# Kernel tuning notes

Measured on AMD Instinct MI355X. Metric: run time of the kernel, lower is better.

## Reference

```python
import jax, jax.numpy as jnp
import numpy as np
import math

IN_FEATURES = 4096
OUT_FEATURES = 4096
TOKENS = 8192


def hydrate_weight(seed, out_features, in_features):
    """Deterministically synthesize the virtual weight matrix from the 64-bit seed.
    Mirrors nn.Linear's kaiming-uniform-style bound (1/sqrt(fan_in)) used by gmem_rs
    hydration; never stored as a parameter."""
    bound = 1.0 / math.sqrt(in_features)
    key = jax.random.key(seed)
    return jax.random.uniform(
        key, (out_features, in_features), dtype=jnp.float32,
        minval=-bound, maxval=bound)


def setup_inputs() -> dict:
    key = jax.random.key(0)
    kx, kb = jax.random.split(key)
    x = jax.random.normal(kx, (TOKENS, IN_FEATURES), dtype=jnp.float32)
    bound = 1.0 / math.sqrt(IN_FEATURES)
    bias = jax.random.uniform(kb, (OUT_FEATURES,), dtype=jnp.float32,
                              minval=-bound, maxval=bound)
    return {"x": x, "bias": bias, "seed": 1140071481}


def reference(x, bias, seed):
    # Hydrate weight on-the-fly from seed (zero-RAM virtual weight), then GEMM.
    W = hydrate_weight(seed, OUT_FEATURES, IN_FEATURES)  # [out, in]
    y = jnp.einsum('ti,oi->to', x, W)  # [tokens, out]
    return y + bias
```

## Files before the change

kernel.cpp:

```cpp
#include <hip/hip_runtime.h>
#include <hip/hip_bf16.h>
#include <stdint.h>

#define TOKENS 8192
#define NOUT   4096
#define KIN    4096

#define BM 256
#define BN 256
#define BK 64
#define NT (KIN / BK)

typedef __attribute__((ext_vector_type(8))) short bf16x8;
typedef __attribute__((ext_vector_type(4))) float f32x4;

__device__ __forceinline__ uint32_t rotl32(uint32_t x, int r) {
  return (x << r) | (x >> (32 - r));
}

__device__ __forceinline__ uint16_t f2bf_rne(float f) {
  uint32_t u = __float_as_uint(f);
  u += 0x7FFFu + ((u >> 16) & 1u);
  return (uint16_t)(u >> 16);
}

__device__ __forceinline__ void threefry2x32(uint32_t k0, uint32_t k1,
                                             uint32_t c0, uint32_t c1,
                                             uint32_t& o0, uint32_t& o1) {
  uint32_t ks2 = 0x1BD11BDAu ^ k0 ^ k1;
  uint32_t x0 = c0 + k0;
  uint32_t x1 = c1 + k1;
#define TFR(r) { x0 += x1; x1 = rotl32(x1, (r)); x1 ^= x0; }
  TFR(13) TFR(15) TFR(26) TFR(6)
  x0 += k1;  x1 += ks2 + 1u;
  TFR(17) TFR(29) TFR(16) TFR(24)
  x0 += ks2; x1 += k0 + 2u;
  TFR(13) TFR(15) TFR(26) TFR(6)
  x0 += k0;  x1 += k1 + 3u;
  TFR(17) TFR(29) TFR(16) TFR(24)
  x0 += k1;  x1 += ks2 + 4u;
  TFR(13) TFR(15) TFR(26) TFR(6)
  x0 += ks2; x1 += k0 + 5u;
#undef TFR
  o0 = x0; o1 = x1;
}

__global__ void prep_kernel(const float* __restrict__ x,
                            uint16_t* __restrict__ xb,
                            uint16_t* __restrict__ W,
                            const int* __restrict__ seed_ptr) {
  uint32_t b = blockIdx.x;
  uint32_t g = b / 3u, r = b % 3u;
  if (r == 0u) {
    uint32_t k1 = (uint32_t)(*seed_ptr);
    uint32_t j0 = (g * 256u + threadIdx.x) * 8u;
    const float scale = 0.03125f;
    const float mn    = -0.015625f;
    union { uint16_t u[8]; bf16x8 v; } rr;
#pragma unroll
    for (int e = 0; e < 8; ++e) {
      uint32_t o0, o1;
      threefry2x32(0u, k1, 0u, j0 + (uint32_t)e, o0, o1);
      uint32_t bits = o0 ^ o1;
      float f = __uint_as_float((bits >> 9) | 0x3F800000u) - 1.0f;
      float v = fmaxf(mn, f * scale + mn);
      rr.u[e] = f2bf_rne(v);
    }
    *(bf16x8*)(W + j0) = rr.v;
  } else {
    uint32_t cg = g * 2u + (r - 1u);
    uint32_t base = (cg * 256u + threadIdx.x) * 8u;
    f32x4 a = __builtin_nontemporal_load((const f32x4*)(x + base));
    f32x4 c = __builtin_nontemporal_load((const f32x4*)(x + base + 4));
    union { uint16_t u[8]; bf16x8 v; } rr;
    rr.u[0] = f2bf_rne(a[0]); rr.u[1] = f2bf_rne(a[1]);
    rr.u[2] = f2bf_rne(a[2]); rr.u[3] = f2bf_rne(a[3]);
    rr.u[4] = f2bf_rne(c[0]); rr.u[5] = f2bf_rne(c[1]);
    rr.u[6] = f2bf_rne(c[2]); rr.u[7] = f2bf_rne(c[3]);
    *(bf16x8*)(xb + base) = rr.v;
  }
}

__global__ __launch_bounds__(512, 2)
void gemm_bias_kernel(const uint16_t* __restrict__ A,
                      const uint16_t* __restrict__ B,
                      const float* __restrict__ bias,
                      float* __restrict__ C) {
  __shared__ uint16_t smem[2][2][16384];

  const int nwgn = NOUT / BN;
  const int nwg  = (TOKENS / BM) * nwgn;
  int bid = blockIdx.x;
  int cpx = nwg >> 3;
  int swzb = (bid & 7) * cpx + (bid >> 3);
  const int tm = (swzb / nwgn) * BM;
  const int tn = (swzb % nwgn) * BN;

  const int t    = threadIdx.x;
  const int lane = t & 63;
  const int wid  = t >> 6;
  const int wm   = wid >> 2;
  const int wn   = wid & 3;
  const int fr   = lane & 15;
  const int fq   = lane >> 4;

  const int swzRd = (lane & 7) << 4;
  const int lsw   = ((lane & 7) ^ (lane >> 3)) << 4;

  const char* sA  = (const char*)(A + (size_t)(tm + wid * 16 + (lane >> 3)) * KIN) + lsw;
  const char* sB  = (const char*)(B + (size_t)(tn + wid * 16 + (lane >> 3)) * KIN) + lsw;
  const char* sA1 = sA + (size_t)128 * KIN * 2;
  const char* sB1 = sB + (size_t)128 * KIN * 2;

  char* const smemB = (char*)&smem[0][0][0];
  char* const dstB  = smemB + wid * 2048 + lane * 16;

  const int rA00 = (wm * 64 + fr) * 128 + ((fq << 4) ^ swzRd);
  const int rA01 = rA00 ^ 64;
  const int rA10 = rA00 + 65536;
  const int rA11 = rA10 ^ 64;
  const int rB00 = 32768 + (wn * 32 + fr) * 128 + ((fq << 4) ^ swzRd);
  const int rB01 = rB00 ^ 64;
  const int rB10 = rB00 + 65536;
  const int rB11 = rB10 ^ 64;

  f32x4 acc[8][4] = {};
  bf16x8 af[2][4], bv0[2][2], bv1[2][2];

  auto stage2 = [&](const char* src, char* dst) {
    __builtin_amdgcn_global_load_lds(
        (const __attribute__((address_space(1))) void*)src,
        (__attribute__((address_space(3))) void*)dst, 16, 0, 0);
    __builtin_amdgcn_global_load_lds(
        (const __attribute__((address_space(1))) void*)(src + (size_t)8 * KIN * 2),
        (__attribute__((address_space(3))) void*)(dst + 1024), 16, 0, 0);
  };

#define VMW(N) asm volatile("s_waitcnt vmcnt(" #N ")" ::: "memory")
#define LKW(N) asm volatile("s_waitcnt lgkmcnt(" #N ")" ::: "memory")
#define SB0    __builtin_amdgcn_sched_barrier(0)
#define PRI(p) __builtin_amdgcn_s_setprio(p)

#define RD_A4(BASE, S)                                                         \
    _Pragma("unroll")                                                          \
    for (int i_ = 0; i_ < 4; ++i_)                                             \
      af[S][i_] = *(const bf16x8*)(smemB + (BASE) + i_ * 2048);

#define RD_B2(BASE, BV, S)                                                     \
    _Pragma("unroll")                                                          \
    for (int j_ = 0; j_ < 2; ++j_)                                             \
      BV[S][j_] = *(const bf16x8*)(smemB + (BASE) + j_ * 2048);

#define MF8(MH, NH, BV, S)                                                     \
    _Pragma("unroll")                                                          \
    for (int i_ = 0; i_ < 4; ++i_)                                             \
      _Pragma("unroll")                                                        \
      for (int j_ = 0; j_ < 2; ++j_)                                           \
        acc[(MH) * 4 + i_][(NH) * 2 + j_] =                                    \
            __builtin_amdgcn_mfma_f32_16x16x32_bf16(                           \
                af[S][i_], BV[S][j_], acc[(MH) * 4 + i_][(NH) * 2 + j_],       \
                0, 0, 0);

#define KTILE(BUF, OFF1, OFF2, MODE)                                           \
  {                                                                            \
                       \
    RD_A4((BUF) ? rA10 : rA00, 0) RD_B2((BUF) ? rB10 : rB00, bv0, 0)           \
    SB0;                                                                       \
    RD_A4((BUF) ? rA11 : rA01, 1) RD_B2((BUF) ? rB11 : rB01, bv0, 1)           \
    if ((MODE) <= 1) stage2(sA1 + (OFF1),                                      \
                            dstB + ((BUF) ^ 1) * 65536 + 16384);               \
    LKW(8);                                                                    \
    __builtin_amdgcn_s_barrier();                                              \
    LKW(6); SB0; PRI(1); MF8(0, 0, bv0, 0)                                     \
    LKW(0); SB0; MF8(0, 0, bv0, 1) PRI(0);                                     \
                                                   \
    RD_B2(((BUF) ? rB10 : rB00) + 16384, bv1, 0)                               \
    SB0;                                                                       \
    RD_B2(((BUF) ? rB11 : rB01) + 16384, bv1, 1)                               \
    LKW(2);                                                                    \
    __builtin_amdgcn_s_barrier();                                              \
    LKW(2); SB0; PRI(1); MF8(0, 1, bv1, 0)                                     \
    LKW(0); SB0; MF8(0, 1, bv1, 1) PRI(0);                                     \
            \
    RD_A4(((BUF) ? rA10 : rA00) + 16384, 0)                                    \
    SB0;                                                                       \
    RD_A4(((BUF) ? rA11 : rA01) + 16384, 1)                                    \
    if ((MODE) == 0) { stage2(sA + (OFF2), dstB + (BUF) * 65536);              \
                       stage2(sB + (OFF2), dstB + (BUF) * 65536 + 32768); }    \
    LKW(4);                                                                    \
    __builtin_amdgcn_s_barrier();                                              \
    LKW(4); SB0; PRI(1); MF8(1, 1, bv1, 0)                                     \
    LKW(0); SB0; MF8(1, 1, bv1, 1) PRI(0);                                     \
        \
    if ((MODE) == 0) stage2(sB1 + (OFF2), dstB + (BUF) * 65536 + 49152);       \
    if ((MODE) == 0) { VMW(6); } else if ((MODE) == 1) { VMW(0); }             \
    __builtin_amdgcn_s_barrier();                                              \
    SB0; PRI(1); MF8(1, 0, bv0, 0) MF8(1, 0, bv0, 1) PRI(0);                   \
  }

  stage2(sA,        dstB);
  stage2(sB,        dstB + 32768);
  stage2(sA1,       dstB + 16384);
  stage2(sB1,       dstB + 49152);
  stage2(sA  + 128, dstB + 65536);
  stage2(sB  + 128, dstB + 65536 + 32768);
  stage2(sB1 + 128, dstB + 65536 + 49152);
  VMW(6);
  __builtin_amdgcn_s_barrier();

  for (int it = 0; it < (NT - 2) / 2; ++it) {
    KTILE(0, 128, 256, 0)
    KTILE(1, 256, 384, 0)
    sA += 256; sB += 256; sA1 += 256; sB1 += 256;
  }
  KTILE(0, 128, 0, 1)
  KTILE(1, 0, 0, 2)

#undef KTILE
#undef MF8
#undef RD_B2
#undef RD_A4
#undef PRI
#undef SB0
#undef LKW
#undef VMW

  __builtin_amdgcn_s_barrier();
  float* const eb = (float*)(smemB + wid * 4608);
  const int erow = lane >> 3;
  const int ecol = (lane & 7) * 4;
#pragma unroll
  for (int mh = 0; mh < 2; ++mh) {
#pragma unroll
    for (int nh = 0; nh < 2; ++nh) {
#pragma unroll
      for (int c = 0; c < 2; ++c) {
#pragma unroll
        for (int i2 = 0; i2 < 2; ++i2)
#pragma unroll
          for (int j = 0; j < 2; ++j)
#pragma unroll
            for (int rr = 0; rr < 4; ++rr)
              eb[(i2 * 16 + fq * 4 + rr) * 36 + j * 16 + fr] =
                  acc[mh * 4 + c * 2 + i2][nh * 2 + j][rr] +
                  bias[tn + wn * 32 + nh * 128 + j * 16 + fr];
        __builtin_amdgcn_s_waitcnt(0);
        const size_t rbase = (size_t)(tm + wm * 64 + mh * 128 + c * 32 + erow);
        float* cp = C + rbase * NOUT + tn + wn * 32 + nh * 128 + ecol;
#pragma unroll
        for (int rb = 0; rb < 4; ++rb) {
          f32x4 v = *(const f32x4*)(eb + (rb * 8 + erow) * 36 + ecol);
          __builtin_nontemporal_store(v, (f32x4*)(cp + (size_t)rb * 8 * NOUT));
        }
        __builtin_amdgcn_s_waitcnt(0);
      }
    }
  }
}

extern "C" void kernel_launch(void* const* d_in, const int* in_sizes, int n_in,
                              void* d_out, int out_size, void* d_ws, size_t ws_size,
                              hipStream_t stream) {
  const float* x    = (const float*)d_in[0];
  const float* bias = (const float*)d_in[1];
  const int*   seed = (const int*)d_in[2];
  float* y = (float*)d_out;

  uint16_t* Wb = (uint16_t*)d_ws;
  uint16_t* Xb = Wb + (size_t)NOUT * KIN;

  prep_kernel<<<24576, 256, 0, stream>>>(x, Xb, Wb, seed);

  const int grid = (TOKENS / BM) * (NOUT / BN);
  gemm_bias_kernel<<<grid, 512, 0, stream>>>(Xb, Wb, bias, y);
}
```

Before: 247.6 us.

## Switch GEMM to 4 waves with 128x128 per-wave tiles and simpler pipeline

Restructures the 256x256 GEMM tile to use 256 threads (4 waves, 2x2) where each wave computes a 128x128 sub-tile with 64 accumulators, instead of 8 waves with 64x64-ish sub-tiles. The staging and compute schedule is simplified: loads are issued in bulk after barriers with full lgkmcnt/vmcnt waits, and the setprio and fine-grained interleaving are dropped. Bias values are hoisted into registers for the epilogue. This raises register pressure heavily (256 accumulator floats per lane) and lowers occupancy, risking spills and less latency hiding.

Measured after the change: 327.9 us. 32.4% more time.

```diff
diff --git a/kernel.cpp b/kernel.cpp
--- a/kernel.cpp
+++ b/kernel.cpp
@@ -81,7 +81,7 @@
   }
 }
 
-__global__ __launch_bounds__(512, 2)
+__global__ __launch_bounds__(256, 1)
 void gemm_bias_kernel(const uint16_t* __restrict__ A,
                       const uint16_t* __restrict__ B,
                       const float* __restrict__ bias,
@@ -99,161 +99,139 @@
   const int t    = threadIdx.x;
   const int lane = t & 63;
   const int wid  = t >> 6;
-  const int wm   = wid >> 2;
-  const int wn   = wid & 3;
+  const int wm   = wid >> 1;
+  const int wn   = wid & 1;
   const int fr   = lane & 15;
   const int fq   = lane >> 4;
 
   const int swzRd = (lane & 7) << 4;
-  const int lsw   = ((lane & 7) ^ (lane >> 3)) << 4;
-
-  const char* sA  = (const char*)(A + (size_t)(tm + wid * 16 + (lane >> 3)) * KIN) + lsw;
-  const char* sB  = (const char*)(B + (size_t)(tn + wid * 16 + (lane >> 3)) * KIN) + lsw;
-  const char* sA1 = sA + (size_t)128 * KIN * 2;
-  const char* sB1 = sB + (size_t)128 * KIN * 2;
+  const int lsw   = ((t & 7) ^ ((t >> 3) & 7)) << 4;
+
+  const char* sA = (const char*)(A + (size_t)(tm + (t >> 3)) * KIN) + lsw;
+  const char* sB = (const char*)(B + (size_t)(tn + (t >> 3)) * KIN) + lsw;
 
   char* const smemB = (char*)&smem[0][0][0];
-  char* const dstB  = smemB + wid * 2048 + lane * 16;
-
-  const int rA00 = (wm * 64 + fr) * 128 + ((fq << 4) ^ swzRd);
-  const int rA01 = rA00 ^ 64;
-  const int rA10 = rA00 + 65536;
-  const int rA11 = rA10 ^ 64;
-  const int rB00 = 32768 + (wn * 32 + fr) * 128 + ((fq << 4) ^ swzRd);
-  const int rB01 = rB00 ^ 64;
-  const int rB10 = rB00 + 65536;
-  const int rB11 = rB10 ^ 64;
-
-  f32x4 acc[8][4] = {};
-  bf16x8 af[2][4], bv0[2][2], bv1[2][2];
-
-  auto stage2 = [&](const char* src, char* dst) {
+  char* const dstT  = smemB + t * 16;
+
+  const int rA0 = (wm * 128 + fr) * 128 + ((fq << 4) ^ swzRd);
+  const int rB0 = 32768 + (wn * 128 + fr) * 128 + ((fq << 4) ^ swzRd);
+
+  f32x4 acc[8][8] = {};
+  bf16x8 af[8], bv[8];
+
+  auto g1 = [&](const char* src, char* dst) {
     __builtin_amdgcn_global_load_lds(
         (const __attribute__((address_space(1))) void*)src,
         (__attribute__((address_space(3))) void*)dst, 16, 0, 0);
-    __builtin_amdgcn_global_load_lds(
-        (const __attribute__((address_space(1))) void*)(src + (size_t)8 * KIN * 2),
-        (__attribute__((address_space(3))) void*)(dst + 1024), 16, 0, 0);
+  };
+  auto stA = [&](int buf, int off) {
+#pragma unroll
+    for (int q = 0; q < 8; ++q)
+      g1(sA + (size_t)q * 262144 + off, dstT + buf * 65536 + q * 4096);
+  };
+  auto stB = [&](int buf, int off, int q0, int q1) {
+#pragma unroll
+    for (int q = 0; q < 8; ++q)
+      if (q >= q0 && q <= q1)
+        g1(sB + (size_t)q * 262144 + off, dstT + buf * 65536 + 32768 + q * 4096);
   };
 
 #define VMW(N) asm volatile("s_waitcnt vmcnt(" #N ")" ::: "memory")
 #define LKW(N) asm volatile("s_waitcnt lgkmcnt(" #N ")" ::: "memory")
 #define SB0    __builtin_amdgcn_sched_barrier(0)
-#define PRI(p) __builtin_amdgcn_s_setprio(p)
-
-#define RD_A4(BASE, S)                                                         \
+
+#define RD_A(BASE)                                                             \
     _Pragma("unroll")                                                          \
-    for (int i_ = 0; i_ < 4; ++i_)                                             \
-      af[S][i_] = *(const bf16x8*)(smemB + (BASE) + i_ * 2048);
-
-#define RD_B2(BASE, BV, S)                                                     \
+    for (int i_ = 0; i_ < 8; ++i_)                                             \
+      af[i_] = *(const bf16x8*)(smemB + (BASE) + i_ * 2048);
+
+#define RD_B(BASE, C0)                                                         \
     _Pragma("unroll")                                                          \
-    for (int j_ = 0; j_ < 2; ++j_)                                             \
-      BV[S][j_] = *(const bf16x8*)(smemB + (BASE) + j_ * 2048);
-
-#define MF8(MH, NH, BV, S)                                                     \
+    for (int c_ = (C0); c_ < (C0) + 4; ++c_)                                   \
+      bv[c_] = *(const bf16x8*)(smemB + (BASE) + c_ * 2048);
+
+#define MF32(C0)                                                               \
     _Pragma("unroll")                                                          \
-    for (int i_ = 0; i_ < 4; ++i_)                                             \
+    for (int i_ = 0; i_ < 8; ++i_)                                             \
       _Pragma("unroll")                                                        \
-      for (int j_ = 0; j_ < 2; ++j_)                                           \
-        acc[(MH) * 4 + i_][(NH) * 2 + j_] =                                    \
-            __builtin_amdgcn_mfma_f32_16x16x32_bf16(                           \
-                af[S][i_], BV[S][j_], acc[(MH) * 4 + i_][(NH) * 2 + j_],       \
-                0, 0, 0);
-
-#define KTILE(BUF, OFF1, OFF2, MODE)                                           \
+      for (int c_ = (C0); c_ < (C0) + 4; ++c_)                                 \
+        acc[i_][c_] = __builtin_amdgcn_mfma_f32_16x16x32_bf16(                 \
+            af[i_], bv[c_], acc[i_][c_], 0, 0, 0);
+
+#define KTILE(BUF, OFF, MODE)                                                  \
   {                                                                            \
-                       \
-    RD_A4((BUF) ? rA10 : rA00, 0) RD_B2((BUF) ? rB10 : rB00, bv0, 0)           \
-    SB0;                                                                       \
-    RD_A4((BUF) ? rA11 : rA01, 1) RD_B2((BUF) ? rB11 : rB01, bv0, 1)           \
-    if ((MODE) <= 1) stage2(sA1 + (OFF1),                                      \
-                            dstB + ((BUF) ^ 1) * 65536 + 16384);               \
-    LKW(8);                                                                    \
-    __builtin_amdgcn_s_barrier();                                              \
-    LKW(6); SB0; PRI(1); MF8(0, 0, bv0, 0)                                     \
-    LKW(0); SB0; MF8(0, 0, bv0, 1) PRI(0);                                     \
-                                                   \
-    RD_B2(((BUF) ? rB10 : rB00) + 16384, bv1, 0)                               \
-    SB0;                                                                       \
-    RD_B2(((BUF) ? rB11 : rB01) + 16384, bv1, 1)                               \
-    LKW(2);                                                                    \
-    __builtin_amdgcn_s_barrier();                                              \
-    LKW(2); SB0; PRI(1); MF8(0, 1, bv1, 0)                                     \
-    LKW(0); SB0; MF8(0, 1, bv1, 1) PRI(0);                                     \
-            \
-    RD_A4(((BUF) ? rA10 : rA00) + 16384, 0)                                    \
-    SB0;                                                                       \
-    RD_A4(((BUF) ? rA11 : rA01) + 16384, 1)                                    \
-    if ((MODE) == 0) { stage2(sA + (OFF2), dstB + (BUF) * 65536);              \
-                       stage2(sB + (OFF2), dstB + (BUF) * 65536 + 32768); }    \
-    LKW(4);                                                                    \
-    __builtin_amdgcn_s_barrier();                                              \
-    LKW(4); SB0; PRI(1); MF8(1, 1, bv1, 0)                                     \
-    LKW(0); SB0; MF8(1, 1, bv1, 1) PRI(0);                                     \
-        \
-    if ((MODE) == 0) stage2(sB1 + (OFF2), dstB + (BUF) * 65536 + 49152);       \
-    if ((MODE) == 0) { VMW(6); } else if ((MODE) == 1) { VMW(0); }             \
-    __builtin_amdgcn_s_barrier();                                              \
-    SB0; PRI(1); MF8(1, 0, bv0, 0) MF8(1, 0, bv0, 1) PRI(0);                   \
-  }
-
-  stage2(sA,        dstB);
-  stage2(sB,        dstB + 32768);
-  stage2(sA1,       dstB + 16384);
-  stage2(sB1,       dstB + 49152);
-  stage2(sA  + 128, dstB + 65536);
-  stage2(sB  + 128, dstB + 65536 + 32768);
-  stage2(sB1 + 128, dstB + 65536 + 49152);
-  VMW(6);
+    const int aB = rA0 + (BUF) * 65536;                                        \
+    const int bB = rB0 + (BUF) * 65536;                                        \
+                                                           \
+    RD_A(aB) RD_B(bB, 0)                                                       \
+    __builtin_amdgcn_s_barrier();                                              \
+    if ((MODE) == 0) { stA((BUF) ^ 1, OFF); stB((BUF) ^ 1, OFF, 0, 3); }       \
+    LKW(0); SB0; MF32(0)                                                       \
+                                                           \
+    RD_B(bB, 4)                                                                \
+    __builtin_amdgcn_s_barrier();                                              \
+    if ((MODE) == 0) stB((BUF) ^ 1, OFF, 4, 7);                                \
+    LKW(0); SB0; MF32(4)                                                       \
+                                     \
+    RD_A(aB ^ 64) RD_B(bB ^ 64, 0)                                             \
+    __builtin_amdgcn_s_barrier();                                              \
+    LKW(0); SB0; MF32(0)                                                       \
+                                \
+    RD_B(bB ^ 64, 4)                                                           \
+    if ((MODE) == 0) VMW(0);                                                   \
+    __builtin_amdgcn_s_barrier();                                              \
+    LKW(0); SB0; MF32(4)                                                       \
+  }
+
+  stA(0, 0); stB(0, 0, 0, 7);
+  VMW(0);
   __builtin_amdgcn_s_barrier();
 
   for (int it = 0; it < (NT - 2) / 2; ++it) {
-    KTILE(0, 128, 256, 0)
-    KTILE(1, 256, 384, 0)
-    sA += 256; sB += 256; sA1 += 256; sB1 += 256;
-  }
-  KTILE(0, 128, 0, 1)
-  KTILE(1, 0, 0, 2)
+    KTILE(0, 128, 0)
+    KTILE(1, 256, 0)
+    sA += 256; sB += 256;
+  }
+  KTILE(0, 128, 0)
+  KTILE(1, 0, 1)
 
 #undef KTILE
-#undef MF8
-#undef RD_B2
-#undef RD_A4
-#undef PRI
+#undef MF32
+#undef RD_B
+#undef RD_A
 #undef SB0
 #undef LKW
 #undef VMW
 
   __builtin_amdgcn_s_barrier();
+  float bb[8];
+#pragma unroll
+  for (int c = 0; c < 8; ++c)
+    bb[c] = bias[tn + wn * 128 + c * 16 + fr];
   float* const eb = (float*)(smemB + wid * 4608);
   const int erow = lane >> 3;
   const int ecol = (lane & 7) * 4;
 #pragma unroll
-  for (int mh = 0; mh < 2; ++mh) {
-#pragma unroll
-    for (int nh = 0; nh < 2; ++nh) {
-#pragma unroll
-      for (int c = 0; c < 2; ++c) {
-#pragma unroll
-        for (int i2 = 0; i2 < 2; ++i2)
-#pragma unroll
-          for (int j = 0; j < 2; ++j)
-#pragma unroll
-            for (int rr = 0; rr < 4; ++rr)
-              eb[(i2 * 16 + fq * 4 + rr) * 36 + j * 16 + fr] =
-                  acc[mh * 4 + c * 2 + i2][nh * 2 + j][rr] +
-                  bias[tn + wn * 32 + nh * 128 + j * 16 + fr];
-        __builtin_amdgcn_s_waitcnt(0);
-        const size_t rbase = (size_t)(tm + wm * 64 + mh * 128 + c * 32 + erow);
-        float* cp = C + rbase * NOUT + tn + wn * 32 + nh * 128 + ecol;
-#pragma unroll
-        for (int rb = 0; rb < 4; ++rb) {
-          f32x4 v = *(const f32x4*)(eb + (rb * 8 + erow) * 36 + ecol);
-          __builtin_nontemporal_store(v, (f32x4*)(cp + (size_t)rb * 8 * NOUT));
-        }
-        __builtin_amdgcn_s_waitcnt(0);
+  for (int cr = 0; cr < 4; ++cr) {
+#pragma unroll
+    for (int cc = 0; cc < 4; ++cc) {
+#pragma unroll
+      for (int i2 = 0; i2 < 2; ++i2)
+#pragma unroll
+        for (int j = 0; j < 2; ++j)
+#pragma unroll
+          for (int rr = 0; rr < 4; ++rr)
+            eb[(i2 * 16 + fq * 4 + rr) * 36 + j * 16 + fr] =
+                acc[cr * 2 + i2][cc * 2 + j][rr] + bb[cc * 2 + j];
+      __builtin_amdgcn_s_waitcnt(0);
+      const size_t rbase = (size_t)(tm + wm * 128 + cr * 32 + erow);
+      float* cp = C + rbase * NOUT + tn + wn * 128 + cc * 32 + ecol;
+#pragma unroll
+      for (int rb = 0; rb < 4; ++rb) {
+        f32x4 v = *(const f32x4*)(eb + (rb * 8 + erow) * 36 + ecol);
+        __builtin_nontemporal_store(v, (f32x4*)(cp + (size_t)rb * 8 * NOUT));
       }
+      __builtin_amdgcn_s_waitcnt(0);
     }
   }
 }
@@ -272,5 +250,5 @@
   prep_kernel<<<24576, 256, 0, stream>>>(x, Xb, Wb, seed);
 
   const int grid = (TOKENS / BM) * (NOUT / BN);
-  gemm_bias_kernel<<<grid, 512, 0, stream>>>(Xb, Wb, bias, y);
-}
+  gemm_bias_kernel<<<grid, 256, 0, stream>>>(Xb, Wb, bias, y);
+}
```
